# Kernel tuning notes

Hardware: AMD Instinct MI355X
Metric: run time of the kernel (lower is better)

Reference implementation:

```python
import math
import jax, jax.numpy as jnp
import numpy as np

B, S, D, H = 2, 2048, 1024, 16
HD = D // H  # head_dim = 64
LN_EPS = 1e-5


def setup_inputs() -> dict:
    key = jax.random.key(0)
    ks = jax.random.split(key, 12)
    scale = 1.0 / math.sqrt(D)
    inp = {
        "x": jax.random.normal(ks[0], (B, S, D), dtype=jnp.float32),
        "cdr_mask": jax.random.uniform(ks[1], (B, 1, S, S), dtype=jnp.float32),
        "Wq": jax.random.normal(ks[2], (D, D), dtype=jnp.float32) * scale,
        "bq": jnp.zeros((D,), dtype=jnp.float32),
        "Wk": jax.random.normal(ks[3], (D, D), dtype=jnp.float32) * scale,
        "bk": jnp.zeros((D,), dtype=jnp.float32),
        "Wv": jax.random.normal(ks[4], (D, D), dtype=jnp.float32) * scale,
        "bv": jnp.zeros((D,), dtype=jnp.float32),
        "Wo": jax.random.normal(ks[5], (D, D), dtype=jnp.float32) * scale,
        "bo": jnp.zeros((D,), dtype=jnp.float32),
        "gamma": jnp.ones((D,), dtype=jnp.float32),
        "beta": jnp.zeros((D,), dtype=jnp.float32),
        "cdr_weight": jnp.float32(1.0),
    }
    return inp


def _rotate_half(t):
    # even / odd interleaved halves, as in the torch module
    t1 = t[..., ::2]
    t2 = t[..., 1::2]
    return jnp.stack((-t2, t1), axis=-1).reshape(t.shape)


def reference(x, cdr_mask, Wq, bq, Wk, bk, Wv, bv, Wo, bo, gamma, beta, cdr_weight):
    b, s, d = x.shape
    # RoPE tables (concatenated, NOT interleaved -- faithful to source)
    inv_freq = 1.0 / (10000.0 ** (jnp.arange(0, HD, 2, dtype=jnp.float32) / HD))
    pos = jnp.arange(s, dtype=jnp.float32)
    sinusoid = pos[:, None] * inv_freq[None, :]          # [S, HD/2]
    sin_pos = jnp.concatenate([jnp.sin(sinusoid)] * 2, axis=-1)[None, None]  # [1,1,S,HD]
    cos_pos = jnp.concatenate([jnp.cos(sinusoid)] * 2, axis=-1)[None, None]

    def proj(W, bias):
        return (x @ W.T + bias).reshape(b, s, H, HD).transpose(0, 2, 1, 3)  # [B,H,S,HD]

    Q = proj(Wq, bq)
    K = proj(Wk, bk)
    V = proj(Wv, bv)
    Q = Q * cos_pos + _rotate_half(Q) * sin_pos
    K = K * cos_pos + _rotate_half(K) * sin_pos

    scores = jnp.einsum('bhqd,bhkd->bhqk', Q, K) / math.sqrt(HD)
    scores = scores + cdr_mask * cdr_weight
    probs = jax.nn.softmax(scores, axis=-1)
    attn = jnp.einsum('bhqk,bhkd->bhqd', probs, V)       # [B,H,S,HD]
    attn = attn.transpose(0, 2, 1, 3).reshape(b, s, d)
    out = attn @ Wo.T + bo                               # dropout is identity at eval

    y = x + out
    mu = jnp.mean(y, axis=-1, keepdims=True)
    var = jnp.var(y, axis=-1, keepdims=True)
    return (y - mu) / jnp.sqrt(var + LN_EPS) * gamma + beta
```

## Files before the change

### kernel.cpp

```cpp
#include <hip/hip_runtime.h>
#include <hip/hip_bf16.h>
#include <math.h>

#define Bn  2
#define Sn  2048
#define Dn  1024
#define Hn  16
#define HDn 64

typedef __attribute__((ext_vector_type(8))) short bf16x8;
typedef __attribute__((ext_vector_type(4))) short bf16x4;
typedef __attribute__((ext_vector_type(4))) float f32x4;

#define LOG2E 1.44269504088896340736f

__device__ __forceinline__ float fexp2(float x) {
    return __builtin_amdgcn_exp2f(x);
}

__device__ __forceinline__ uint2 pack4bf(float a, float b, float c, float d) {
    union { __hip_bfloat162 h2[2]; uint2 u; } p;
    p.h2[0] = __float22bfloat162_rn(make_float2(a, b));
    p.h2[1] = __float22bfloat162_rn(make_float2(c, d));
    return p.u;
}

__device__ __forceinline__ bf16x4 pack4bfv(float a, float b, float c, float d) {
    union { __hip_bfloat162 h2[2]; bf16x4 v; } p;
    p.h2[0] = __float22bfloat162_rn(make_float2(a, b));
    p.h2[1] = __float22bfloat162_rn(make_float2(c, d));
    return p.v;
}

__device__ __forceinline__ void g2l16(const void* g, void* lbase) {
    __builtin_amdgcn_global_load_lds(
        (const __attribute__((address_space(1))) void*)g,
        (__attribute__((address_space(3))) void*)lbase, 16, 0, 0);
}

__global__ __launch_bounds__(256) void prep_kernel(
    const float* __restrict__ x,
    const float* __restrict__ Wq, const float* __restrict__ Wk,
    const float* __restrict__ Wv, const float* __restrict__ Wo,
    __hip_bfloat16* __restrict__ Xb,
    __hip_bfloat16* __restrict__ Wqb, __hip_bfloat16* __restrict__ Wkb,
    __hip_bfloat16* __restrict__ Wvb, __hip_bfloat16* __restrict__ Wob,
    float2* __restrict__ CS)
{
    const int bx = blockIdx.x, tid = threadIdx.x;
    if (bx < 4096) {
        const size_t i = (size_t)bx * 1024 + tid * 4;
        float4 v = *(const float4*)(x + i);
        *(uint2*)(Xb + i) = pack4bf(v.x, v.y, v.z, v.w);
    } else if (bx < 8192) {
        const int r = bx - 4096;
        const int which = r >> 10;
        const size_t i = (size_t)(r & 1023) * 1024 + tid * 4;
        const float* s = (which == 0) ? Wq : (which == 1) ? Wk : (which == 2) ? Wv : Wo;
        __hip_bfloat16* d = (which == 0) ? Wqb : (which == 1) ? Wkb : (which == 2) ? Wvb : Wob;
        float4 v = *(const float4*)(s + i);
        *(uint2*)(d + i) = pack4bf(v.x, v.y, v.z, v.w);
    } else {
        const float NEG_L2C = -0.41524101186092033f;
        const int idx = ((bx - 8192) * 256 + tid) * 2;
        const int s = idx >> 6, d0 = idx & 63;
        const float sf = (float)s;
        const float f0 = exp2f((float)(d0 & 31) * NEG_L2C);
        const float f1 = exp2f((float)((d0 + 1) & 31) * NEG_L2C);
        *(float4*)(&CS[(size_t)s * 64 + d0]) =
            make_float4(__cosf(sf * f0), __sinf(sf * f0),
                        __cosf(sf * f1), __sinf(sf * f1));
    }
}

__global__ __launch_bounds__(256) void qkv_proj(
    const __hip_bfloat16* __restrict__ X,
    const __hip_bfloat16* __restrict__ Wqb, const __hip_bfloat16* __restrict__ Wkb,
    const __hip_bfloat16* __restrict__ Wvb,
    const float* __restrict__ bq, const float* __restrict__ bk,
    const float* __restrict__ bv,
    const float2* __restrict__ CS,
    __hip_bfloat16* __restrict__ Qo, __hip_bfloat16* __restrict__ Ko,
    __hip_bfloat16* __restrict__ Vo)
{
    __shared__ __hip_bfloat16 Xs[128 * 64];
    __shared__ __hip_bfloat16 Ws[128 * 64];
    const int tid  = threadIdx.x;
    const int w    = tid >> 6, lane = tid & 63;
    const int lrow = lane & 15, lhi = lane >> 4;
    const int L    = blockIdx.x;
    const int xcd  = L & 7, slot = L >> 3;
    const int wq   = slot >> 2, ms = slot & 3;
    const int pj   = wq >> 3;
    const int n0   = (wq & 7) * 128;
    const int m0   = (xcd + 8 * ms) * 128;
    const int rm   = (w & 1) * 64;
    const int rn   = (w >> 1) * 64;
    const int srow = lane >> 3, scb = lane & 7;

    const __hip_bfloat16* Wb   = (pj == 0) ? Wqb : (pj == 1) ? Wkb : Wvb;
    const float*          bias = (pj == 0) ? bq : (pj == 1) ? bk : bv;

    f32x4 acc[16];
#pragma unroll
    for (int i = 0; i < 16; i++) acc[i] = (f32x4){0.f, 0.f, 0.f, 0.f};

    for (int k0 = 0; k0 < Dn; k0 += 64) {
#pragma unroll
        for (int j = 0; j < 4; j++) {
            const int row = w * 32 + j * 8 + srow;
            const int sc  = ((scb ^ (row & 7)) << 3);
            g2l16(X  + (size_t)(m0 + row) * Dn + k0 + sc, &Xs[(w * 32 + j * 8) * 64]);
            g2l16(Wb + (size_t)(n0 + row) * Dn + k0 + sc, &Ws[(w * 32 + j * 8) * 64]);
        }
        __syncthreads();

#pragma unroll
        for (int ksub = 0; ksub < 2; ksub++) {
            bf16x8 FX[4], FW[4];
#pragma unroll
            for (int t = 0; t < 4; t++) {
                const int ra = rm + t * 16 + lrow;
                FX[t] = *(const bf16x8*)&Xs[ra * 64 + (((ksub * 4 + lhi) ^ (ra & 7)) << 3)];
                const int rb = rn + t * 16 + lrow;
                FW[t] = *(const bf16x8*)&Ws[rb * 64 + (((ksub * 4 + lhi) ^ (rb & 7)) << 3)];
            }
            if (pj == 2) {
#pragma unroll
                for (int tm = 0; tm < 4; tm++)
#pragma unroll
                    for (int tn = 0; tn < 4; tn++)
                        acc[tm * 4 + tn] = __builtin_amdgcn_mfma_f32_16x16x32_bf16(
                            FX[tm], FW[tn], acc[tm * 4 + tn], 0, 0, 0);
            } else {
#pragma unroll
                for (int tn = 0; tn < 4; tn++)
#pragma unroll
                    for (int tm = 0; tm < 4; tm++)
                        acc[tn * 4 + tm] = __builtin_amdgcn_mfma_f32_16x16x32_bf16(
                            FW[tn], FX[tm], acc[tn * 4 + tm], 0, 0, 0);
            }
        }
        __syncthreads();
    }

    const int h = (n0 >> 6) + (w >> 1);

    if (pj != 2) {
        __hip_bfloat16* outb = (pj == 0) ? Qo : Ko;
        const float SCL = 0.125f * LOG2E;
#pragma unroll
        for (int tn = 0; tn < 4; tn++) {
            const int hd0 = tn * 16 + lhi * 4;
            const float4 b4 = *(const float4*)&bias[n0 + rn + hd0];
#pragma unroll
            for (int tm = 0; tm < 4; tm++) {
                const int m = m0 + rm + tm * 16 + lrow;
                const int s = m & (Sn - 1), bb = m >> 11;
                f32x4 a = acc[tn * 4 + tm];
                float v0 = a[0] + b4.x, v1 = a[1] + b4.y;
                float v2 = a[2] + b4.z, v3 = a[3] + b4.w;
                if (pj == 0) { v0 *= SCL; v1 *= SCL; v2 *= SCL; v3 *= SCL; }
                const float4 cs01 = *(const float4*)&CS[(size_t)s * 64 + hd0];
                const float4 cs23 = *(const float4*)&CS[(size_t)s * 64 + hd0 + 2];
                const float r0 = v0 * cs01.x - v1 * cs01.y;
                const float r1 = v1 * cs01.z + v0 * cs01.w;
                const float r2 = v2 * cs23.x - v3 * cs23.y;
                const float r3 = v3 * cs23.z + v2 * cs23.w;
                *(uint2*)(outb + ((size_t)(bb * Hn + h) * Sn + s) * HDn + hd0) =
                    pack4bf(r0, r1, r2, r3);
            }
        }
    } else {
#pragma unroll
        for (int tn = 0; tn < 4; tn++) {
            const int c = tn * 16 + lrow;
            const float bc = bias[n0 + rn + c];
#pragma unroll
            for (int tm = 0; tm < 4; tm++) {
                const int mb = m0 + rm + tm * 16 + lhi * 4;
                const int s = mb & (Sn - 1), bb = mb >> 11;
                f32x4 a = acc[tm * 4 + tn];
                *(uint2*)(Vo + ((size_t)(bb * Hn + h) * HDn + c) * Sn + s) =
                    pack4bf(a[0] + bc, a[1] + bc, a[2] + bc, a[3] + bc);
            }
        }
    }
}

__global__ __launch_bounds__(256) void o_proj(
    const __hip_bfloat16* __restrict__ X,
    const __hip_bfloat16* __restrict__ Wb,
    const float* __restrict__ bias,
    const float* __restrict__ resid,
    float* __restrict__ outf)
{
    __shared__ __hip_bfloat16 Xs[128 * 64];
    __shared__ __hip_bfloat16 Ws[128 * 64];
    const int tid  = threadIdx.x;
    const int w    = tid >> 6, lane = tid & 63;
    const int lrow = lane & 15, lhi = lane >> 4;
    const int L    = blockIdx.x;
    const int xcd  = L & 7, slot = L >> 3;
    const int n0   = (slot >> 2) * 128;
    const int m0   = (xcd + 8 * (slot & 3)) * 128;
    const int rm   = (w & 1) * 64;
    const int rn   = (w >> 1) * 64;
    const int srow = lane >> 3, scb = lane & 7;

    f32x4 acc[16];
#pragma unroll
    for (int i = 0; i < 16; i++) acc[i] = (f32x4){0.f, 0.f, 0.f, 0.f};

    for (int k0 = 0; k0 < Dn; k0 += 64) {
#pragma unroll
        for (int j = 0; j < 4; j++) {
            const int row = w * 32 + j * 8 + srow;
            const int sc  = ((scb ^ (row & 7)) << 3);
            g2l16(X  + (size_t)(m0 + row) * Dn + k0 + sc, &Xs[(w * 32 + j * 8) * 64]);
            g2l16(Wb + (size_t)(n0 + row) * Dn + k0 + sc, &Ws[(w * 32 + j * 8) * 64]);
        }
        __syncthreads();

#pragma unroll
        for (int ksub = 0; ksub < 2; ksub++) {
            bf16x8 FX[4], FW[4];
#pragma unroll
            for (int t = 0; t < 4; t++) {
                const int ra = rm + t * 16 + lrow;
                FX[t] = *(const bf16x8*)&Xs[ra * 64 + (((ksub * 4 + lhi) ^ (ra & 7)) << 3)];
                const int rb = rn + t * 16 + lrow;
                FW[t] = *(const bf16x8*)&Ws[rb * 64 + (((ksub * 4 + lhi) ^ (rb & 7)) << 3)];
            }
#pragma unroll
            for (int tn = 0; tn < 4; tn++)
#pragma unroll
                for (int tm = 0; tm < 4; tm++)
                    acc[tn * 4 + tm] = __builtin_amdgcn_mfma_f32_16x16x32_bf16(
                        FW[tn], FX[tm], acc[tn * 4 + tm], 0, 0, 0);
        }
        __syncthreads();
    }

#pragma unroll
    for (int tn = 0; tn < 4; tn++) {
        const int nb = n0 + rn + tn * 16 + lhi * 4;
        const float4 b4 = *(const float4*)&bias[nb];
#pragma unroll
        for (int tm = 0; tm < 4; tm++) {
            const int m = m0 + rm + tm * 16 + lrow;
            f32x4 a = acc[tn * 4 + tm];
            const float4 rr = *(const float4*)&resid[(size_t)m * Dn + nb];
            *(float4*)(outf + (size_t)m * Dn + nb) =
                make_float4(a[0] + b4.x + rr.x, a[1] + b4.y + rr.y,
                            a[2] + b4.z + rr.z, a[3] + b4.w + rr.w);
        }
    }
}

struct __align__(16) TileBuf {
    __hip_bfloat16 K[64 * 64];
    __hip_bfloat16 V[64 * 64];
    float          M[64 * 64];
};

__device__ __forceinline__ void stage_tiles(
    TileBuf& t,
    const __hip_bfloat16* __restrict__ Kb,
    const __hip_bfloat16* __restrict__ Vb,
    const float* __restrict__ Mq0,
    int k0, int w, int lane)
{
#pragma unroll
    for (int j = 0; j < 2; j++) {
        const int row = w * 16 + j * 8 + (lane >> 3);
        const int blk = (lane & 7) ^ (row & 7);
        g2l16(Kb + (size_t)(k0 + row) * HDn + blk * 8, &t.K[(w * 16 + j * 8) * 64]);
        g2l16(Vb + (size_t)row * Sn + k0 + blk * 8,    &t.V[(w * 16 + j * 8) * 64]);
    }
#pragma unroll
    for (int j = 0; j < 4; j++) {
        const int row = w * 16 + j * 4 + (lane >> 4);
        const int blk = (lane & 15) ^ (row & 7);
        g2l16(Mq0 + (size_t)row * Sn + k0 + blk * 4,   &t.M[(w * 16 + j * 4) * 64]);
    }
}

__global__ __launch_bounds__(256) void attn_kernel(
    const __hip_bfloat16* __restrict__ Q,
    const __hip_bfloat16* __restrict__ K,
    const __hip_bfloat16* __restrict__ Vt,
    const float* __restrict__ mask,
    const float* __restrict__ cwp,
    __hip_bfloat16* __restrict__ A)
{
    __shared__ TileBuf tb[2];
    const int tid  = threadIdx.x;
    const int w    = tid >> 6, lane = tid & 63;
    const int lrow = lane & 15, lhi = lane >> 4;
    const int L    = blockIdx.x;
    const int xcd  = L & 7, slot = L >> 3;
    const int b    = xcd >> 2;
    const int h    = (xcd & 3) * 4 + (slot & 3);
    const int q0   = (slot >> 2) * 64;
    const int bh   = b * Hn + h;
    const int q    = q0 + w * 16 + lrow;
    const float cwl = cwp[0] * LOG2E;

    const __hip_bfloat16* Qp  = Q + ((size_t)bh * Sn + q) * HDn + lhi * 8;
    const bf16x8 Qf0 = *(const bf16x8*)(Qp);
    const bf16x8 Qf1 = *(const bf16x8*)(Qp + 32);
    const __hip_bfloat16* Kb  = K  + (size_t)bh * Sn * HDn;
    const __hip_bfloat16* Vb  = Vt + (size_t)bh * HDn * Sn;
    const float*          Mq0 = mask + ((size_t)b * Sn + q0) * Sn;

    f32x4 Oc[4];
#pragma unroll
    for (int i = 0; i < 4; i++) Oc[i] = (f32x4){0.f, 0.f, 0.f, 0.f};
    float lsum = 0.f;

    stage_tiles(tb[0], Kb, Vb, Mq0, 0, w, lane);
    __syncthreads();

    for (int it = 0; it < Sn / 64; it++) {
        const int k0 = it * 64;
        if (it + 1 < Sn / 64)
            stage_tiles(tb[(it + 1) & 1], Kb, Vb, Mq0, k0 + 64, w, lane);
        const TileBuf& t = tb[it & 1];

        f32x4 st[4];
#pragma unroll
        for (int kt = 0; kt < 4; kt++) {
            const int rl = kt * 16 + lrow;
            const bf16x8 ka = *(const bf16x8*)&t.K[rl * 64 + ((lhi       ^ (rl & 7)) * 8)];
            const bf16x8 kc = *(const bf16x8*)&t.K[rl * 64 + (((4 + lhi) ^ (rl & 7)) * 8)];
            f32x4 z = (f32x4){0.f, 0.f, 0.f, 0.f};
            z = __builtin_amdgcn_mfma_f32_16x16x32_bf16(ka, Qf0, z, 0, 0, 0);
            z = __builtin_amdgcn_mfma_f32_16x16x32_bf16(kc, Qf1, z, 0, 0, 0);
            st[kt] = z;
        }

        const int rq = w * 16 + lrow;
        bf16x4 pk[4];
#pragma unroll
        for (int kt = 0; kt < 4; kt++) {
            const int mb = (kt * 4 + lhi) ^ (rq & 7);
            const f32x4 mf = *(const f32x4*)&t.M[rq * 64 + mb * 4];
            const float p0 = fexp2(fmaf(mf[0], cwl, st[kt][0]));
            const float p1 = fexp2(fmaf(mf[1], cwl, st[kt][1]));
            const float p2 = fexp2(fmaf(mf[2], cwl, st[kt][2]));
            const float p3 = fexp2(fmaf(mf[3], cwl, st[kt][3]));
            lsum += (p0 + p1) + (p2 + p3);
            pk[kt] = pack4bfv(p0, p1, p2, p3);
        }

#pragma unroll
        for (int ch = 0; ch < 4; ch++) {
            const int rv = ch * 16 + lrow;
#pragma unroll
            for (int kt = 0; kt < 4; kt++) {
                const int eo = (((2 * kt + (lhi >> 1)) ^ (rv & 7)) * 8) + (lhi & 1) * 4;
                const bf16x4 vf = *(const bf16x4*)&t.V[rv * 64 + eo];
                Oc[ch] = __builtin_amdgcn_mfma_f32_16x16x16bf16_1k(
                    vf, pk[kt], Oc[ch], 0, 0, 0);
            }
        }
        __syncthreads();
    }

    lsum += __shfl_xor(lsum, 16, 64);
    lsum += __shfl_xor(lsum, 32, 64);
    const float inv = 1.f / lsum;

    __hip_bfloat16* ap = A + ((size_t)(b * Sn + q)) * Dn + h * HDn;
#pragma unroll
    for (int ch = 0; ch < 4; ch++) {
        *(uint2*)(ap + ch * 16 + lhi * 4) =
            pack4bf(Oc[ch][0] * inv, Oc[ch][1] * inv, Oc[ch][2] * inv, Oc[ch][3] * inv);
    }
}

__global__ __launch_bounds__(256) void ln_kernel(
    const float* __restrict__ Yin, const float* __restrict__ gamma,
    const float* __restrict__ beta, float* __restrict__ out)
{
    __shared__ float2 wred[4];
    const int m   = blockIdx.x;
    const int tid = threadIdx.x;
    const size_t base = (size_t)m * Dn + tid * 4;
    float4 y = *(const float4*)(Yin + base);

    float s1 = y.x + y.y + y.z + y.w;
    float s2 = y.x * y.x + y.y * y.y + y.z * y.z + y.w * y.w;
#pragma unroll
    for (int off = 32; off; off >>= 1) {
        s1 += __shfl_xor(s1, off, 64);
        s2 += __shfl_xor(s2, off, 64);
    }
    if ((tid & 63) == 0) wred[tid >> 6] = make_float2(s1, s2);
    __syncthreads();
    const float S1 = wred[0].x + wred[1].x + wred[2].x + wred[3].x;
    const float S2 = wred[0].y + wred[1].y + wred[2].y + wred[3].y;
    const float mu  = S1 * (1.f / Dn);
    const float var = S2 * (1.f / Dn) - mu * mu;
    const float rin = rsqrtf(var + 1e-5f);

    float4 gv = *(const float4*)(gamma + tid * 4);
    float4 bv = *(const float4*)(beta  + tid * 4);
    *(float4*)(out + base) = make_float4((y.x - mu) * rin * gv.x + bv.x,
                                         (y.y - mu) * rin * gv.y + bv.y,
                                         (y.z - mu) * rin * gv.z + bv.z,
                                         (y.w - mu) * rin * gv.w + bv.w);
}

extern "C" void kernel_launch(void* const* d_in, const int* in_sizes, int n_in,
                              void* d_out, int out_size, void* d_ws, size_t ws_size,
                              hipStream_t stream)
{
    const float* x     = (const float*)d_in[0];
    const float* mask  = (const float*)d_in[1];
    const float* Wq    = (const float*)d_in[2];
    const float* bq    = (const float*)d_in[3];
    const float* Wk    = (const float*)d_in[4];
    const float* bk    = (const float*)d_in[5];
    const float* Wv    = (const float*)d_in[6];
    const float* bv    = (const float*)d_in[7];
    const float* Wo    = (const float*)d_in[8];
    const float* bo    = (const float*)d_in[9];
    const float* gamma = (const float*)d_in[10];
    const float* beta  = (const float*)d_in[11];
    const float* cw    = (const float*)d_in[12];
    float* out = (float*)d_out;

    const size_t MB = 1024 * 1024;
    char* ws = (char*)d_ws;
    __hip_bfloat16* Xb  = (__hip_bfloat16*)(ws);
    __hip_bfloat16* Qb  = (__hip_bfloat16*)(ws +  8 * MB);
    __hip_bfloat16* Kb  = (__hip_bfloat16*)(ws + 16 * MB);
    __hip_bfloat16* Vtb = (__hip_bfloat16*)(ws + 24 * MB);
    __hip_bfloat16* Wqb = (__hip_bfloat16*)(ws + 32 * MB);
    __hip_bfloat16* Wkb = (__hip_bfloat16*)(ws + 34 * MB);
    __hip_bfloat16* Wvb = (__hip_bfloat16*)(ws + 36 * MB);
    __hip_bfloat16* Wob = (__hip_bfloat16*)(ws + 38 * MB);
    float2*         CS  = (float2*)        (ws + 40 * MB);
    __hip_bfloat16* Ab  = Xb;

    prep_kernel<<<8448, 256, 0, stream>>>(x, Wq, Wk, Wv, Wo,
                                          Xb, Wqb, Wkb, Wvb, Wob, CS);
    qkv_proj<<<768, 256, 0, stream>>>(Xb, Wqb, Wkb, Wvb,
                                      bq, bk, bv, CS, Qb, Kb, Vtb);
    attn_kernel<<<1024, 256, 0, stream>>>(Qb, Kb, Vtb, mask, cw, Ab);
    o_proj<<<256, 256, 0, stream>>>(Ab, Wob, bo, x, out);
    ln_kernel<<<Bn * Sn, 256, 0, stream>>>(out, gamma, beta, out);
}
```

Measured before the change: 283.9 us.

## Split-K the output projection and compute softmax row sums via MFMA

The output projection now splits K in two across 512 blocks instead of 256, writing two fp32 partial outputs that the LayerNorm kernel sums; bias and residual are added only in the first partial. The attention kernel replaces the scalar row-sum and cross-lane shuffles with an extra MFMA against a ones vector on the bf16 probabilities. The workspace is rearranged so the partial buffers reuse the Q/K/V region. The aim is better CU occupancy for the small projection GEMM and fewer VALU adds in attention, at the cost of extra fp32 traffic and a row sum computed from bf16-rounded probabilities.

Result: no change. 279.4 us (-1.6%).

```diff
diff --git a/kernel.cpp b/kernel.cpp
--- a/kernel.cpp
+++ b/kernel.cpp
@@ -193,7 +193,7 @@
     const __hip_bfloat16* __restrict__ Wb,
     const float* __restrict__ bias,
     const float* __restrict__ resid,
-    float* __restrict__ outf)
+    float* __restrict__ opart)
 {
     __shared__ __hip_bfloat16 Xs[128 * 64];
     __shared__ __hip_bfloat16 Ws[128 * 64];
@@ -202,8 +202,10 @@
     const int lrow = lane & 15, lhi = lane >> 4;
     const int L    = blockIdx.x;
     const int xcd  = L & 7, slot = L >> 3;
-    const int n0   = (slot >> 2) * 128;
     const int m0   = (xcd + 8 * (slot & 3)) * 128;
+    const int n0   = ((slot >> 2) & 7) * 128;
+    const int ks   = slot >> 5;
+    const int kbeg = ks * 512;
     const int rm   = (w & 1) * 64;
     const int rn   = (w >> 1) * 64;
     const int srow = lane >> 3, scb = lane & 7;
@@ -212,7 +214,7 @@
 #pragma unroll
     for (int i = 0; i < 16; i++) acc[i] = (f32x4){0.f, 0.f, 0.f, 0.f};
 
-    for (int k0 = 0; k0 < Dn; k0 += 64) {
+    for (int k0 = kbeg; k0 < kbeg + 512; k0 += 64) {
 #pragma unroll
         for (int j = 0; j < 4; j++) {
             const int row = w * 32 + j * 8 + srow;
@@ -242,18 +244,22 @@
         __syncthreads();
     }
 
+    float* outp = opart + (size_t)ks * Bn * Sn * Dn;
 #pragma unroll
     for (int tn = 0; tn < 4; tn++) {
         const int nb = n0 + rn + tn * 16 + lhi * 4;
-        const float4 b4 = *(const float4*)&bias[nb];
+        float4 b4 = make_float4(0.f, 0.f, 0.f, 0.f);
+        if (ks == 0) b4 = *(const float4*)&bias[nb];
 #pragma unroll
         for (int tm = 0; tm < 4; tm++) {
             const int m = m0 + rm + tm * 16 + lrow;
             f32x4 a = acc[tn * 4 + tm];
-            const float4 rr = *(const float4*)&resid[(size_t)m * Dn + nb];
-            *(float4*)(outf + (size_t)m * Dn + nb) =
-                make_float4(a[0] + b4.x + rr.x, a[1] + b4.y + rr.y,
-                            a[2] + b4.z + rr.z, a[3] + b4.w + rr.w);
+            float4 o = make_float4(a[0] + b4.x, a[1] + b4.y, a[2] + b4.z, a[3] + b4.w);
+            if (ks == 0) {
+                const float4 rr = *(const float4*)&resid[(size_t)m * Dn + nb];
+                o.x += rr.x; o.y += rr.y; o.z += rr.z; o.w += rr.w;
+            }
+            *(float4*)(outp + (size_t)m * Dn + nb) = o;
         }
     }
 }
@@ -307,6 +313,9 @@
     const int q    = q0 + w * 16 + lrow;
     const float cwl = cwp[0] * LOG2E;
 
+    const short ONE = (short)0x3F80;
+    const bf16x4 ones = (bf16x4){ONE, ONE, ONE, ONE};
+
     const __hip_bfloat16* Qp  = Q + ((size_t)bh * Sn + q) * HDn + lhi * 8;
     const bf16x8 Qf0 = *(const bf16x8*)(Qp);
     const bf16x8 Qf1 = *(const bf16x8*)(Qp + 32);
@@ -317,7 +326,7 @@
     f32x4 Oc[4];
 #pragma unroll
     for (int i = 0; i < 4; i++) Oc[i] = (f32x4){0.f, 0.f, 0.f, 0.f};
-    float lsum = 0.f;
+    f32x4 Sc = (f32x4){0.f, 0.f, 0.f, 0.f};
 
     stage_tiles(tb[0], Kb, Vb, Mq0, 0, w, lane);
     __syncthreads();
@@ -350,8 +359,8 @@
             const float p1 = fexp2(fmaf(mf[1], cwl, st[kt][1]));
             const float p2 = fexp2(fmaf(mf[2], cwl, st[kt][2]));
             const float p3 = fexp2(fmaf(mf[3], cwl, st[kt][3]));
-            lsum += (p0 + p1) + (p2 + p3);
             pk[kt] = pack4bfv(p0, p1, p2, p3);
+            Sc = __builtin_amdgcn_mfma_f32_16x16x16bf16_1k(ones, pk[kt], Sc, 0, 0, 0);
         }
 
 #pragma unroll
@@ -368,9 +377,7 @@
         __syncthreads();
     }
 
-    lsum += __shfl_xor(lsum, 16, 64);
-    lsum += __shfl_xor(lsum, 32, 64);
-    const float inv = 1.f / lsum;
+    const float inv = 1.f / Sc[0];
 
     __hip_bfloat16* ap = A + ((size_t)(b * Sn + q)) * Dn + h * HDn;
 #pragma unroll
@@ -381,14 +388,17 @@
 }
 
 __global__ __launch_bounds__(256) void ln_kernel(
-    const float* __restrict__ Yin, const float* __restrict__ gamma,
-    const float* __restrict__ beta, float* __restrict__ out)
+    const float* __restrict__ Yin0, const float* __restrict__ Yin1,
+    const float* __restrict__ gamma, const float* __restrict__ beta,
+    float* __restrict__ out)
 {
     __shared__ float2 wred[4];
     const int m   = blockIdx.x;
     const int tid = threadIdx.x;
     const size_t base = (size_t)m * Dn + tid * 4;
-    float4 y = *(const float4*)(Yin + base);
+    float4 y0 = *(const float4*)(Yin0 + base);
+    float4 y1 = *(const float4*)(Yin1 + base);
+    float4 y = make_float4(y0.x + y1.x, y0.y + y1.y, y0.z + y1.z, y0.w + y1.w);
 
     float s1 = y.x + y.y + y.z + y.w;
     float s2 = y.x * y.x + y.y * y.y + y.z * y.z + y.w * y.w;
@@ -435,14 +445,15 @@
     const size_t MB = 1024 * 1024;
     char* ws = (char*)d_ws;
     __hip_bfloat16* Xb  = (__hip_bfloat16*)(ws);
-    __hip_bfloat16* Qb  = (__hip_bfloat16*)(ws +  8 * MB);
-    __hip_bfloat16* Kb  = (__hip_bfloat16*)(ws + 16 * MB);
-    __hip_bfloat16* Vtb = (__hip_bfloat16*)(ws + 24 * MB);
-    __hip_bfloat16* Wqb = (__hip_bfloat16*)(ws + 32 * MB);
-    __hip_bfloat16* Wkb = (__hip_bfloat16*)(ws + 34 * MB);
-    __hip_bfloat16* Wvb = (__hip_bfloat16*)(ws + 36 * MB);
-    __hip_bfloat16* Wob = (__hip_bfloat16*)(ws + 38 * MB);
-    float2*         CS  = (float2*)        (ws + 40 * MB);
+    __hip_bfloat16* Wob = (__hip_bfloat16*)(ws +  8 * MB);
+    __hip_bfloat16* Wqb = (__hip_bfloat16*)(ws + 10 * MB);
+    __hip_bfloat16* Wkb = (__hip_bfloat16*)(ws + 12 * MB);
+    __hip_bfloat16* Wvb = (__hip_bfloat16*)(ws + 14 * MB);
+    float2*         CS  = (float2*)        (ws + 16 * MB);
+    __hip_bfloat16* Qb  = (__hip_bfloat16*)(ws + 17 * MB);
+    __hip_bfloat16* Kb  = (__hip_bfloat16*)(ws + 25 * MB);
+    __hip_bfloat16* Vtb = (__hip_bfloat16*)(ws + 33 * MB);
+    float*          opart = (float*)       (ws + 17 * MB);
     __hip_bfloat16* Ab  = Xb;
 
     prep_kernel<<<8448, 256, 0, stream>>>(x, Wq, Wk, Wv, Wo,
@@ -450,6 +461,7 @@
     qkv_proj<<<768, 256, 0, stream>>>(Xb, Wqb, Wkb, Wvb,
                                       bq, bk, bv, CS, Qb, Kb, Vtb);
     attn_kernel<<<1024, 256, 0, stream>>>(Qb, Kb, Vtb, mask, cw, Ab);
-    o_proj<<<256, 256, 0, stream>>>(Ab, Wob, bo, x, out);
-    ln_kernel<<<Bn * Sn, 256, 0, stream>>>(out, gamma, beta, out);
-}
+    o_proj<<<512, 256, 0, stream>>>(Ab, Wob, bo, x, opart);
+    ln_kernel<<<Bn * Sn, 256, 0, stream>>>(opart, opart + (size_t)Bn * Sn * Dn,
+                                           gamma, beta, out);
+}
```
